# Performance work log

Measured on AMD Instinct MI355X. Metric: run time of the kernel, lower is better.

## Reference

```python
import jax, jax.numpy as jnp
import numpy as np

LEAKY = 0.1

def _leaky(x):
    return jax.nn.leaky_relu(x, LEAKY)

def _gather(pts, idx):
    # pts: [B, M, C], idx: [B, N, K] -> [B, N, K, C]
    return jax.vmap(lambda p, i: p[i])(pts, idx)

def _cross(xyz1, xyz2, p1, p2, pos_w, pos_b, mlps, k):
    # xyz1:[B,N1,3] xyz2:[B,N2,3] p1:[B,N1,D] p2:[B,N2,D]
    d = (jnp.sum(xyz1 * xyz1, -1)[:, :, None]
         + jnp.sum(xyz2 * xyz2, -1)[:, None, :]
         - 2.0 * jnp.einsum('bnc,bmc->bnm', xyz1, xyz2))  # [B,N1,N2]
    _, idx = jax.lax.top_k(-d, k)                          # smallest-k -> [B,N1,K]
    nb_xyz = _gather(xyz2, idx)                            # [B,N1,K,3]
    direction = nb_xyz - xyz1[:, :, None, :]
    g2 = _gather(p2, idx)                                  # [B,N1,K,D]
    posf = direction @ pos_w.T + pos_b                     # 1x1 conv on 3->D
    x = _leaky(g2 + p1[:, :, None, :] + posf)              # bn = Identity
    for w, b in mlps:
        x = _leaky(x @ w.T + b)                            # 1x1 Conv2d + bias + leaky
    return jnp.max(x, axis=2)                              # max-pool over K -> [B,N1,Cout]

def setup_inputs() -> dict:
    key = jax.random.key(0)
    ks = jax.random.split(key, 24)
    B, N, C, M1, M2, K = 2, 8192, 64, 64, 64, 16
    s = 0.1
    inp = {
        'pc1': jax.random.normal(ks[0], (B, 3, N), jnp.float32),
        'pc2': jax.random.normal(ks[1], (B, 3, N), jnp.float32),
        'feat1': jax.random.normal(ks[2], (B, C, N), jnp.float32),
        'feat2': jax.random.normal(ks[3], (B, C, N), jnp.float32),
        't11_w': jax.random.normal(ks[4], (M1, C), jnp.float32) * s,
        't11_b': jax.random.normal(ks[5], (M1,), jnp.float32) * s,
        't22_w': jax.random.normal(ks[6], (M1, C), jnp.float32) * s,
        't22_b': jax.random.normal(ks[7], (M1,), jnp.float32) * s,
        'pos1_w': jax.random.normal(ks[8], (M1, 3), jnp.float32) * s,
        'pos1_b': jax.random.normal(ks[9], (M1,), jnp.float32) * s,
        'mlp1_w1': jax.random.normal(ks[10], (M1, M1), jnp.float32) * s,
        'mlp1_b1': jax.random.normal(ks[11], (M1,), jnp.float32) * s,
        'mlp1_w2': jax.random.normal(ks[12], (M1, M1), jnp.float32) * s,
        'mlp1_b2': jax.random.normal(ks[13], (M1,), jnp.float32) * s,
        't1_w': jax.random.normal(ks[14], (M2, M1), jnp.float32) * s,
        't1_b': jax.random.normal(ks[15], (M2,), jnp.float32) * s,
        't2_w': jax.random.normal(ks[16], (M2, M1), jnp.float32) * s,
        't2_b': jax.random.normal(ks[17], (M2,), jnp.float32) * s,
        'pos2_w': jax.random.normal(ks[18], (M2, 3), jnp.float32) * s,
        'pos2_b': jax.random.normal(ks[19], (M2,), jnp.float32) * s,
        'mlp2_w1': jax.random.normal(ks[20], (M2, M2), jnp.float32) * s,
        'mlp2_b1': jax.random.normal(ks[21], (M2,), jnp.float32) * s,
    }
    return inp

def reference(pc1, pc2, feat1, feat2,
              t11_w, t11_b, t22_w, t22_b,
              pos1_w, pos1_b, mlp1_w1, mlp1_b1, mlp1_w2, mlp1_b2,
              t1_w, t1_b, t2_w, t2_b,
              pos2_w, pos2_b, mlp2_w1, mlp2_b1):
    K = 16
    x1 = jnp.transpose(pc1, (0, 2, 1))    # [B,N,3]
    x2 = jnp.transpose(pc2, (0, 2, 1))
    f1 = jnp.transpose(feat1, (0, 2, 1))  # [B,N,C]
    f2 = jnp.transpose(feat2, (0, 2, 1))
    mlp1 = [(mlp1_w1, mlp1_b1), (mlp1_w2, mlp1_b2)]
    mlp2 = [(mlp2_w1, mlp2_b1)]
    # feat1_new = cross_t1(cross(pc1, pc2, t11(feat1), t22(feat2), pos1, mlp1))
    q1 = f1 @ t11_w.T + t11_b
    q2 = f2 @ t22_w.T + t22_b
    fn1 = _cross(x1, x2, q1, q2, pos1_w, pos1_b, mlp1, K) @ t1_w.T + t1_b  # [B,N,M2]
    # feat2_new = cross_t2(cross(pc2, pc1, t11(feat2), t22(feat1), pos1, mlp1))
    r1 = f2 @ t11_w.T + t11_b
    r2 = f1 @ t22_w.T + t22_b
    fn2 = _cross(x2, x1, r1, r2, pos1_w, pos1_b, mlp1, K) @ t2_w.T + t2_b  # [B,N,M2]
    # feat1_final = cross(pc1, pc2, feat1_new, feat2_new, pos2, mlp2)
    ff = _cross(x1, x2, fn1, fn2, pos2_w, pos2_b, mlp2, K)                 # [B,N,M2]
    to_cn = lambda a: jnp.transpose(a, (0, 2, 1))  # back to [B,C,N] torch layout
    return (to_cn(fn1), to_cn(fn2), to_cn(ff))
```

## Files before the change

kernel.cpp:

```cpp
#include <hip/hip_runtime.h>

#define NPTS 8192
#define BATCH 2
#define CC 64
#define KNN 16

typedef __attribute__((ext_vector_type(4))) float  f32x4;
typedef __attribute__((ext_vector_type(8))) short  s16x8;
typedef unsigned short u16;

__device__ __forceinline__ u16 f2bf(float f) {
  unsigned u = __float_as_uint(f);
  unsigned r = ((u >> 16) & 1u) + 0x7FFFu;
  return (u16)((u + r) >> 16);
}

__device__ __forceinline__ float leaky(float v) { return fmaxf(v, 0.1f * v); }

__device__ __forceinline__ s16x8 pack8(const float v[8]) {
  union { s16x8 v8; u16 s[8]; } u;
  #pragma unroll
  for (int j = 0; j < 8; ++j) u.s[j] = f2bf(v[j]);
  return u.v8;
}

__global__ __launch_bounds__(256) void kprep(const float* __restrict__ pc1,
                                             const float* __restrict__ pc2,
                                             float4* __restrict__ x1t,
                                             float4* __restrict__ x2t) {
  int i = blockIdx.x * 256 + threadIdx.x;
  int b = i >> 13, n = i & (NPTS - 1);
  size_t base = (size_t)b * 3 * NPTS + n;
  float x = pc1[base], y = pc1[base + NPTS], z = pc1[base + 2 * NPTS];
  x1t[i] = make_float4(x, y, z, x * x + y * y + z * z);
  x = pc2[base]; y = pc2[base + NPTS]; z = pc2[base + 2 * NPTS];
  x2t[i] = make_float4(x, y, z, x * x + y * y + z * z);
}

__global__ __launch_bounds__(256) void ktrans(
    const float* __restrict__ f1, const float* __restrict__ f2,
    const float* __restrict__ w11, const float* __restrict__ b11,
    const float* __restrict__ w22, const float* __restrict__ b22,
    float* __restrict__ q1, float* __restrict__ q2,
    float* __restrict__ r1, float* __restrict__ r2) {
  const int z = blockIdx.z;
  const float* in = (z == 0 || z == 3) ? f1 : f2;
  const float* W  = (z == 0 || z == 2) ? w11 : w22;
  const float* Bb = (z == 0 || z == 2) ? b11 : b22;
  float* out = (z == 0) ? q1 : (z == 1) ? q2 : (z == 2) ? r1 : r2;
  const int b = blockIdx.y;
  const int n0 = blockIdx.x * 64;
  const int t = threadIdx.x;

  __shared__ float ft[64 * 65];
  __shared__ float wt[64 * 68];

  #pragma unroll
  for (int j = 0; j < 16; ++j) {
    int e = t + 256 * j;
    int c = e >> 6, tn = e & 63;
    ft[c * 65 + tn] = in[((size_t)b * 64 + c) * NPTS + n0 + tn];
  }
  #pragma unroll
  for (int j = 0; j < 16; ++j) {
    int e = t + 256 * j;
    int mm = e >> 6, c = e & 63;
    wt[c * 68 + mm] = W[e];
  }
  __syncthreads();

  const int tn = t & 63, mg = t >> 6;
  float a[16];
  #pragma unroll
  for (int u = 0; u < 4; ++u) {
    float4 bb = *(const float4*)&Bb[16 * mg + 4 * u];
    a[4 * u] = bb.x; a[4 * u + 1] = bb.y; a[4 * u + 2] = bb.z; a[4 * u + 3] = bb.w;
  }
  for (int c = 0; c < 64; ++c) {
    float x = ft[c * 65 + tn];
    #pragma unroll
    for (int u = 0; u < 4; ++u) {
      float4 w4 = *(const float4*)&wt[c * 68 + 16 * mg + 4 * u];
      a[4 * u]     = fmaf(x, w4.x, a[4 * u]);
      a[4 * u + 1] = fmaf(x, w4.y, a[4 * u + 1]);
      a[4 * u + 2] = fmaf(x, w4.z, a[4 * u + 2]);
      a[4 * u + 3] = fmaf(x, w4.w, a[4 * u + 3]);
    }
  }
  size_t ob = ((size_t)b * NPTS + n0 + tn) * 64 + 16 * mg;
  #pragma unroll
  for (int u = 0; u < 4; ++u)
    *(float4*)&out[ob + 4 * u] =
        make_float4(a[4 * u], a[4 * u + 1], a[4 * u + 2], a[4 * u + 3]);
}

__device__ __forceinline__ void kinsert(unsigned key, unsigned ii,
                                        unsigned (&D)[16], unsigned (&I)[16]) {
  if (key < D[15]) {
    bool lt[16];
    #pragma unroll
    for (int j = 0; j < 16; ++j) lt[j] = key < D[j];
    #pragma unroll
    for (int j = 15; j >= 1; --j) {
      D[j] = lt[j - 1] ? D[j - 1] : (lt[j] ? key : D[j]);
      I[j] = lt[j - 1] ? I[j - 1] : (lt[j] ? ii  : I[j]);
    }
    if (lt[0]) { D[0] = key; I[0] = ii; }
  }
}

#define CHUNKS 8
#define CHSZ (NPTS / CHUNKS)
#define NCOLD 2

#define ARD 20
#define ART 12

__global__ __launch_bounds__(256) void kknnA(const float4* __restrict__ x1t,
                                             const float4* __restrict__ x2t,
                                             uint2* __restrict__ part) {
  const int dir = blockIdx.z;
  const int b = blockIdx.y;
  const float4* xq = dir ? x2t : x1t;
  const float4* xc = dir ? x1t : x2t;
  const int t = threadIdx.x;
  const int qb = blockIdx.x & 31;
  const int ck = blockIdx.x >> 5;
  const int qi = qb * 256 + t;

  __shared__ float4 tile[CHSZ];
  __shared__ uint2 ring[ARD][256];

  const float4* src = xc + (size_t)b * NPTS + ck * CHSZ;
  #pragma unroll
  for (int j = 0; j < CHSZ / 256; ++j) tile[j * 256 + t] = src[j * 256 + t];

  float4 Q = xq[(size_t)b * NPTS + qi];
  const float nqx = -2.f * Q.x, nqy = -2.f * Q.y, nqz = -2.f * Q.z, qn = Q.w;

  unsigned D[16], I[16];
  #pragma unroll
  for (int j = 0; j < 16; ++j) { D[j] = 0xFFFFFFFFu; I[j] = 0u; }

  __syncthreads();

  const unsigned ibase = (unsigned)(ck * CHSZ);
  #pragma unroll
  for (int j = 0; j < 16; ++j) {
    float4 C = tile[j];
    float d = fmaf(C.x, nqx, fmaf(C.y, nqy, fmaf(C.z, nqz, qn + C.w)));
    unsigned key = (unsigned)max((int)__float_as_uint(d), 0);
    kinsert(key, ibase + j, D, I);
  }

  int cnt = 0;
  for (int j0 = 16; j0 < CHSZ; j0 += 8) {
    unsigned D15 = D[15];
    #pragma unroll
    for (int u = 0; u < 8; ++u) {
      float4 C = tile[j0 + u];
      float d = fmaf(C.x, nqx, fmaf(C.y, nqy, fmaf(C.z, nqz, qn + C.w)));
      unsigned key = (unsigned)max((int)__float_as_uint(d), 0);
      ring[cnt][t] = make_uint2(key, ibase + j0 + u);
      cnt += (key < D15) ? 1 : 0;
    }
    if (__any(cnt >= ART)) {
      for (int e = 0; e < cnt; ++e) {
        uint2 kv = ring[e][t];
        kinsert(kv.x, kv.y, D, I);
      }
      cnt = 0;
    }
  }
  for (int e = 0; e < cnt; ++e) {
    uint2 kv = ring[e][t];
    kinsert(kv.x, kv.y, D, I);
  }

  uint2* pb = part + ((size_t)(((dir << 1) | b) * CHUNKS + ck) * 16) * NPTS;
  #pragma unroll
  for (int j = 0; j < 16; ++j)
    pb[(size_t)j * NPTS + qi] = make_uint2(D[j], I[j]);
}

#define BRD 24
#define BRT 16

__global__ __launch_bounds__(256) void kknnB(const float4* __restrict__ x1t,
                                             const float4* __restrict__ x2t,
                                             uint2* __restrict__ part) {
  const int dir = blockIdx.z;
  const int b = blockIdx.y;
  const float4* xq = dir ? x2t : x1t;
  const float4* xc = dir ? x1t : x2t;
  const int t = threadIdx.x;
  const int qb = blockIdx.x & 31;
  const int ck = NCOLD + (blockIdx.x >> 5);
  const int qi = qb * 256 + t;

  __shared__ float4 tile[CHSZ];
  __shared__ u16 ring[BRD][256];

  const float4* src = xc + (size_t)b * NPTS + ck * CHSZ;
  #pragma unroll
  for (int j = 0; j < CHSZ / 256; ++j) tile[j * 256 + t] = src[j * 256 + t];

  float4 Q = xq[(size_t)b * NPTS + qi];
  const float nqx = -2.f * Q.x, nqy = -2.f * Q.y, nqz = -2.f * Q.z, qn = Q.w;

  const size_t gb = (size_t)(((dir << 1) | b) * CHUNKS) * 16 * NPTS;
  unsigned ta = part[gb + (size_t)15 * NPTS + qi].x;
  unsigned tb = part[gb + (size_t)(16 + 15) * NPTS + qi].x;
  const unsigned tfB = min(ta, tb) + 1u;

  unsigned D[16], I[16];
  #pragma unroll
  for (int j = 0; j < 16; ++j) { D[j] = 0xFFFFFFFFu; I[j] = 0u; }
  int cnt = 0;

  __syncthreads();

  const unsigned ibase = (unsigned)(ck * CHSZ);
  for (int j0 = 0; j0 < CHSZ; j0 += 8) {
    unsigned w = min(D[15], tfB);
    #pragma unroll
    for (int u = 0; u < 8; ++u) {
      float4 C = tile[j0 + u];
      float d = fmaf(C.x, nqx, fmaf(C.y, nqy, fmaf(C.z, nqz, qn + C.w)));
      unsigned key = (unsigned)max((int)__float_as_uint(d), 0);
      ring[cnt][t] = (u16)(j0 + u);
      cnt += (key < w) ? 1 : 0;
    }
    if (__any(cnt >= BRT)) {
      for (int e = 0; e < cnt; ++e) {
        int ji = ring[e][t];
        float4 C = tile[ji];
        float d = fmaf(C.x, nqx, fmaf(C.y, nqy, fmaf(C.z, nqz, qn + C.w)));
        unsigned key = (unsigned)max((int)__float_as_uint(d), 0);
        kinsert(key, ibase + ji, D, I);
      }
      cnt = 0;
    }
  }
  for (int e = 0; e < cnt; ++e) {
    int ji = ring[e][t];
    float4 C = tile[ji];
    float d = fmaf(C.x, nqx, fmaf(C.y, nqy, fmaf(C.z, nqz, qn + C.w)));
    unsigned key = (unsigned)max((int)__float_as_uint(d), 0);
    kinsert(key, ibase + ji, D, I);
  }

  uint2* pb = part + ((size_t)(((dir << 1) | b) * CHUNKS + ck) * 16) * NPTS;
  #pragma unroll
  for (int j = 0; j < 16; ++j)
    pb[(size_t)j * NPTS + qi] = make_uint2(D[j], I[j]);
}

__global__ __launch_bounds__(256) void kmerge(const uint2* __restrict__ part,
                                              int* __restrict__ idx12,
                                              int* __restrict__ idx21) {
  const int dir = blockIdx.z, b = blockIdx.y;
  const int qi = blockIdx.x * 256 + threadIdx.x;
  const uint2* pb = part + ((size_t)(((dir << 1) | b) * CHUNKS) * 16) * NPTS;

  unsigned D[16], I[16];
  #pragma unroll
  for (int j = 0; j < 16; ++j) {
    uint2 kv = pb[(size_t)j * NPTS + qi];
    D[j] = kv.x; I[j] = kv.y;
  }
  for (int ck = 1; ck < CHUNKS; ++ck) {
    #pragma unroll
    for (int j = 0; j < 16; ++j) {
      uint2 kv = pb[(size_t)(ck * 16 + j) * NPTS + qi];
      kinsert(kv.x, kv.y, D, I);
    }
  }
  int* out = dir ? idx21 : idx12;
  size_t ob = ((size_t)b * NPTS + qi) * 16;
  #pragma unroll
  for (int j = 0; j < 16; ++j) out[ob + j] = (int)I[j];
}

template <int NL>
__global__ __launch_bounds__(256) void kcross(
    const float4* __restrict__ xq0, const float4* __restrict__ xc0, const int* __restrict__ idx0,
    const float* __restrict__ p10, const float* __restrict__ p20,
    float* __restrict__ orm0, float* __restrict__ ocn0,
    const float4* __restrict__ xq1, const float4* __restrict__ xc1, const int* __restrict__ idx1,
    const float* __restrict__ p11, const float* __restrict__ p21,
    float* __restrict__ orm1, float* __restrict__ ocn1,
    const float* __restrict__ posw, const float* __restrict__ posb,
    const float* __restrict__ w1, const float* __restrict__ b1,
    const float* __restrict__ w2, const float* __restrict__ b2) {
  const float4* xq; const float4* xc; const int* idx; const float* p1; const float* p2;
  float* orm; float* ocn;
  if (blockIdx.y == 0) { xq = xq0; xc = xc0; idx = idx0; p1 = p10; p2 = p20; orm = orm0; ocn = ocn0; }
  else                 { xq = xq1; xc = xc1; idx = idx1; p1 = p11; p2 = p21; orm = orm1; ocn = ocn1; }

  __shared__ float4 pw4[64];
  __shared__ __align__(16) u16 ylds[4][16 * 72];

  const int t = threadIdx.x;
  const int lane = t & 63;
  const int w = t >> 6;
  const int m = lane & 15;
  const int q = lane >> 4;

  if (t < 64) pw4[t] = make_float4(posw[t * 3], posw[t * 3 + 1], posw[t * 3 + 2], posb[t]);
  __syncthreads();

  s16x8 wf[2][4][2];
  float bv[2][4];
  #pragma unroll
  for (int l = 0; l < NL; ++l) {
    const float* Wl = l ? w2 : w1;
    const float* Bl = l ? b2 : b1;
    #pragma unroll
    for (int ct = 0; ct < 4; ++ct) {
      bv[l][ct] = Bl[16 * ct + m];
      const float* rowp = Wl + (size_t)(16 * ct + m) * 64;
      #pragma unroll
      for (int kt = 0; kt < 2; ++kt) {
        const float* pp = rowp + 32 * kt + 8 * q;
        float4 A  = *(const float4*)pp;
        float4 Bq = *(const float4*)(pp + 4);
        float vv[8] = {A.x, A.y, A.z, A.w, Bq.x, Bq.y, Bq.z, Bq.w};
        wf[l][ct][kt] = pack8(vv);
      }
    }
  }

  u16* yw = &ylds[w][0];
  const f32x4 zz = {0.f, 0.f, 0.f, 0.f};

  #pragma unroll 1
  for (int i = 0; i < 4; ++i) {
    int gp = blockIdx.x * 16 + w * 4 + i;
    int b = gp >> 13, n = gp & (NPTS - 1);
    size_t qb = (size_t)b * NPTS + n;
    int nb = idx[qb * 16 + m];
    size_t cb = (size_t)b * NPTS + nb;
    float4 qp  = xq[qb];
    float4 nbp = xc[cb];
    float dx = nbp.x - qp.x, dy = nbp.y - qp.y, dz = nbp.z - qp.z;

    s16x8 af[2];
    #pragma unroll
    for (int h = 0; h < 2; ++h) {
      int c0 = 32 * h + 8 * q;
      const float* g2p = p2 + cb * 64 + c0;
      float4 ga = *(const float4*)g2p;
      float4 gb = *(const float4*)(g2p + 4);
      const float* p1p = p1 + qb * 64 + c0;
      float4 pa = *(const float4*)p1p;
      float4 pb = *(const float4*)(p1p + 4);
      float gg[8] = {ga.x + pa.x, ga.y + pa.y, ga.z + pa.z, ga.w + pa.w,
                     gb.x + pb.x, gb.y + pb.y, gb.z + pb.z, gb.w + pb.w};
      float vv[8];
      #pragma unroll
      for (int j = 0; j < 8; ++j) {
        float4 pw = pw4[c0 + j];
        float v = gg[j] + pw.w;
        v = fmaf(dx, pw.x, v);
        v = fmaf(dy, pw.y, v);
        v = fmaf(dz, pw.z, v);
        vv[j] = leaky(v);
      }
      af[h] = pack8(vv);
    }

    f32x4 acc[4];
    #pragma unroll
    for (int ct = 0; ct < 4; ++ct) {
      acc[ct] = __builtin_amdgcn_mfma_f32_16x16x32_bf16(af[0], wf[0][ct][0], zz, 0, 0, 0);
      acc[ct] = __builtin_amdgcn_mfma_f32_16x16x32_bf16(af[1], wf[0][ct][1], acc[ct], 0, 0, 0);
    }
    float y[4][4];
    #pragma unroll
    for (int ct = 0; ct < 4; ++ct)
      #pragma unroll
      for (int r = 0; r < 4; ++r)
        y[ct][r] = leaky(acc[ct][r] + bv[0][ct]);

    if (NL == 2) {
      #pragma unroll
      for (int ct = 0; ct < 4; ++ct)
        #pragma unroll
        for (int r = 0; r < 4; ++r)
          yw[(q * 4 + r) * 72 + 16 * ct + m] = f2bf(y[ct][r]);
      asm volatile("s_waitcnt lgkmcnt(0)" ::: "memory");
      s16x8 a2[2];
      a2[0] = *(const s16x8*)(yw + m * 72 + 8 * q);
      a2[1] = *(const s16x8*)(yw + m * 72 + 32 + 8 * q);
      #pragma unroll
      for (int ct = 0; ct < 4; ++ct) {
        acc[ct] = __builtin_amdgcn_mfma_f32_16x16x32_bf16(a2[0], wf[1][ct][0], zz, 0, 0, 0);
        acc[ct] = __builtin_amdgcn_mfma_f32_16x16x32_bf16(a2[1], wf[1][ct][1], acc[ct], 0, 0, 0);
      }
      #pragma unroll
      for (int ct = 0; ct < 4; ++ct)
        #pragma unroll
        for (int r = 0; r < 4; ++r)
          y[ct][r] = leaky(acc[ct][r] + bv[1][ct]);
      asm volatile("s_waitcnt lgkmcnt(0)" ::: "memory");
    }

    float pm[4];
    #pragma unroll
    for (int ct = 0; ct < 4; ++ct) {
      float v = fmaxf(fmaxf(y[ct][0], y[ct][1]), fmaxf(y[ct][2], y[ct][3]));
      v = fmaxf(v, __shfl_xor(v, 16));
      v = fmaxf(v, __shfl_xor(v, 32));
      pm[ct] = v;
    }
    float sel = (q == 0) ? pm[0] : (q == 1) ? pm[1] : (q == 2) ? pm[2] : pm[3];
    if (orm) orm[qb * 64 + lane] = sel;
    if (ocn) ocn[((size_t)b * 64 + lane) * NPTS + n] = sel;
  }
}

__global__ __launch_bounds__(256) void kpost(
    const float* __restrict__ inA, const float* __restrict__ inB,
    const float* __restrict__ wA, const float* __restrict__ bA,
    const float* __restrict__ wB, const float* __restrict__ bB,
    float* __restrict__ frA, float* __restrict__ frB,
    float* __restrict__ cnA, float* __restrict__ cnB) {
  const int z = blockIdx.z;
  const float* in = z ? inB : inA;
  const float* W  = z ? wB : wA;
  const float* Bb = z ? bB : bA;
  float* fr = z ? frB : frA;
  float* cn = z ? cnB : cnA;
  const int b = blockIdx.y;
  const int n0 = blockIdx.x * 64;
  const int t = threadIdx.x;

  __shared__ float pl[64 * 65];
  __shared__ float wt[64 * 68];

  #pragma unroll
  for (int j = 0; j < 16; ++j) {
    int e = t + 256 * j;
    int r = e >> 6, c = e & 63;
    pl[r * 65 + c] = in[((size_t)b * NPTS + n0 + r) * 64 + c];
  }
  #pragma unroll
  for (int j = 0; j < 16; ++j) {
    int e = t + 256 * j;
    int mm = e >> 6, c = e & 63;
    wt[c * 68 + mm] = W[e];
  }
  __syncthreads();

  const int tn = t & 63, mg = t >> 6;
  float a[16];
  #pragma unroll
  for (int u = 0; u < 4; ++u) {
    float4 bb = *(const float4*)&Bb[16 * mg + 4 * u];
    a[4 * u] = bb.x; a[4 * u + 1] = bb.y; a[4 * u + 2] = bb.z; a[4 * u + 3] = bb.w;
  }
  for (int c = 0; c < 64; ++c) {
    float x = pl[tn * 65 + c];
    #pragma unroll
    for (int u = 0; u < 4; ++u) {
      float4 w4 = *(const float4*)&wt[c * 68 + 16 * mg + 4 * u];
      a[4 * u]     = fmaf(x, w4.x, a[4 * u]);
      a[4 * u + 1] = fmaf(x, w4.y, a[4 * u + 1]);
      a[4 * u + 2] = fmaf(x, w4.z, a[4 * u + 2]);
      a[4 * u + 3] = fmaf(x, w4.w, a[4 * u + 3]);
    }
  }
  size_t ob = ((size_t)b * NPTS + n0 + tn) * 64 + 16 * mg;
  #pragma unroll
  for (int u = 0; u < 4; ++u)
    *(float4*)&fr[ob + 4 * u] =
        make_float4(a[4 * u], a[4 * u + 1], a[4 * u + 2], a[4 * u + 3]);
  #pragma unroll
  for (int jj = 0; jj < 16; ++jj) {
    int mo = 16 * mg + jj;
    cn[((size_t)b * 64 + mo) * NPTS + n0 + tn] = a[jj];
  }
}

extern "C" void kernel_launch(void* const* d_in, const int* in_sizes, int n_in,
                              void* d_out, int out_size, void* d_ws, size_t ws_size,
                              hipStream_t stream) {
  const float* pc1   = (const float*)d_in[0];
  const float* pc2   = (const float*)d_in[1];
  const float* feat1 = (const float*)d_in[2];
  const float* feat2 = (const float*)d_in[3];
  const float* t11w  = (const float*)d_in[4];
  const float* t11b  = (const float*)d_in[5];
  const float* t22w  = (const float*)d_in[6];
  const float* t22b  = (const float*)d_in[7];
  const float* pos1w = (const float*)d_in[8];
  const float* pos1b = (const float*)d_in[9];
  const float* m1w1  = (const float*)d_in[10];
  const float* m1b1  = (const float*)d_in[11];
  const float* m1w2  = (const float*)d_in[12];
  const float* m1b2  = (const float*)d_in[13];
  const float* t1w   = (const float*)d_in[14];
  const float* t1b   = (const float*)d_in[15];
  const float* t2w   = (const float*)d_in[16];
  const float* t2b   = (const float*)d_in[17];
  const float* pos2w = (const float*)d_in[18];
  const float* pos2b = (const float*)d_in[19];
  const float* m2w1  = (const float*)d_in[20];
  const float* m2b1  = (const float*)d_in[21];

  char* ws = (char*)d_ws;
  size_t off = 0;
  auto take = [&](size_t bytes) {
    char* p = ws + off;
    off += (bytes + 255) & ~(size_t)255;
    return p;
  };
  float4* x1t  = (float4*)take((size_t)BATCH * NPTS * sizeof(float4));
  float4* x2t  = (float4*)take((size_t)BATCH * NPTS * sizeof(float4));
  int* idx12   = (int*)take((size_t)BATCH * NPTS * KNN * 4);
  int* idx21   = (int*)take((size_t)BATCH * NPTS * KNN * 4);
  float* q1    = (float*)take((size_t)BATCH * NPTS * CC * 4);
  float* q2    = (float*)take((size_t)BATCH * NPTS * CC * 4);
  float* r1    = (float*)take((size_t)BATCH * NPTS * CC * 4);
  float* r2    = (float*)take((size_t)BATCH * NPTS * CC * 4);
  float* poolA = (float*)take((size_t)BATCH * NPTS * CC * 4);
  float* poolB = (float*)take((size_t)BATCH * NPTS * CC * 4);
  float* fn1   = (float*)take((size_t)BATCH * NPTS * CC * 4);
  float* fn2   = (float*)take((size_t)BATCH * NPTS * CC * 4);
  take((size_t)2 * 1024 * 1024);
  uint2* part  = (uint2*)q1;

  float* out = (float*)d_out;
  size_t seg = (size_t)BATCH * CC * NPTS;

  kprep<<<dim3(BATCH * NPTS / 256), 256, 0, stream>>>(pc1, pc2, x1t, x2t);
  kknnA<<<dim3(32 * NCOLD, BATCH, 2), 256, 0, stream>>>(x1t, x2t, part);
  kknnB<<<dim3(32 * (CHUNKS - NCOLD), BATCH, 2), 256, 0, stream>>>(x1t, x2t, part);
  kmerge<<<dim3(NPTS / 256, BATCH, 2), 256, 0, stream>>>(part, idx12, idx21);
  ktrans<<<dim3(NPTS / 64, BATCH, 4), 256, 0, stream>>>(
      feat1, feat2, t11w, t11b, t22w, t22b, q1, q2, r1, r2);
  kcross<2><<<dim3(1024, 2), 256, 0, stream>>>(
      x1t, x2t, idx12, q1, q2, poolA, (float*)nullptr,
      x2t, x1t, idx21, r1, r2, poolB, (float*)nullptr,
      pos1w, pos1b, m1w1, m1b1, m1w2, m1b2);
  kpost<<<dim3(NPTS / 64, BATCH, 2), 256, 0, stream>>>(
      poolA, poolB, t1w, t1b, t2w, t2b, fn1, fn2, out, out + seg);
  kcross<1><<<dim3(1024, 1), 256, 0, stream>>>(
      x1t, x2t, idx12, fn1, fn2, (float*)nullptr, out + 2 * seg,
      x1t, x2t, idx12, fn1, fn2, (float*)nullptr, (float*)nullptr,
      pos2w, pos2b, m2w1, m2b1, m2w1, m2b1);
}
```

Before: 463.6 us.

## Split cold KNN pass into smaller sub-chunks and stage final cross output via LDS

The first-pass KNN now uses four 512-point sub-chunks instead of two 1024-point chunks, and drops the serial 16-insert warmup. The second pass covers the remaining six 1024-point chunks and filters with a threshold taken from the minimum of four cold lists. The goal is more parallelism in the latency-bound cold pass at the cost of more partial lists for the merge to read. Separately, the final cross kernel stages its channel-major output in shared memory so it can write coalesced float4 stores instead of scattered scalars.

```diff
diff --git a/kernel.cpp b/kernel.cpp
--- a/kernel.cpp
+++ b/kernel.cpp
@@ -109,14 +109,78 @@
   }
 }
 
-#define CHUNKS 8
-#define CHSZ (NPTS / CHUNKS)
-#define NCOLD 2
-
-#define ARD 20
-#define ART 12
+#define ASUB 4
+#define ASZ 512
+#define WCH 6
+#define WSZ 1024
+#define NLISTS (ASUB + WCH)
+
+#define ARD 24
+#define ART 16
 
 __global__ __launch_bounds__(256) void kknnA(const float4* __restrict__ x1t,
+                                             const float4* __restrict__ x2t,
+                                             uint2* __restrict__ part) {
+  const int dir = blockIdx.z;
+  const int b = blockIdx.y;
+  const float4* xq = dir ? x2t : x1t;
+  const float4* xc = dir ? x1t : x2t;
+  const int t = threadIdx.x;
+  const int qb = blockIdx.x & 31;
+  const int sc = blockIdx.x >> 5;
+  const int qi = qb * 256 + t;
+
+  __shared__ float4 tile[ASZ];
+  __shared__ uint2 ring[ARD][256];
+
+  const float4* src = xc + (size_t)b * NPTS + sc * ASZ;
+  #pragma unroll
+  for (int j = 0; j < ASZ / 256; ++j) tile[j * 256 + t] = src[j * 256 + t];
+
+  float4 Q = xq[(size_t)b * NPTS + qi];
+  const float nqx = -2.f * Q.x, nqy = -2.f * Q.y, nqz = -2.f * Q.z, qn = Q.w;
+
+  unsigned D[16], I[16];
+  #pragma unroll
+  for (int j = 0; j < 16; ++j) { D[j] = 0xFFFFFFFFu; I[j] = 0u; }
+  int cnt = 0;
+
+  __syncthreads();
+
+  const unsigned ibase = (unsigned)(sc * ASZ);
+  for (int j0 = 0; j0 < ASZ; j0 += 8) {
+    unsigned D15 = D[15];
+    #pragma unroll
+    for (int u = 0; u < 8; ++u) {
+      float4 C = tile[j0 + u];
+      float d = fmaf(C.x, nqx, fmaf(C.y, nqy, fmaf(C.z, nqz, qn + C.w)));
+      unsigned key = (unsigned)max((int)__float_as_uint(d), 0);
+      ring[cnt][t] = make_uint2(key, ibase + j0 + u);
+      cnt += (key < D15) ? 1 : 0;
+    }
+    if (__any(cnt >= ART)) {
+      for (int e = 0; e < cnt; ++e) {
+        uint2 kv = ring[e][t];
+        kinsert(kv.x, kv.y, D, I);
+      }
+      cnt = 0;
+    }
+  }
+  for (int e = 0; e < cnt; ++e) {
+    uint2 kv = ring[e][t];
+    kinsert(kv.x, kv.y, D, I);
+  }
+
+  uint2* pb = part + ((size_t)(((dir << 1) | b) * NLISTS + sc) * 16) * NPTS;
+  #pragma unroll
+  for (int j = 0; j < 16; ++j)
+    pb[(size_t)j * NPTS + qi] = make_uint2(D[j], I[j]);
+}
+
+#define BRD 24
+#define BRT 16
+
+__global__ __launch_bounds__(256) void kknnB(const float4* __restrict__ x1t,
                                              const float4* __restrict__ x2t,
                                              uint2* __restrict__ part) {
   const int dir = blockIdx.z;
@@ -127,91 +191,24 @@
   const int qb = blockIdx.x & 31;
   const int ck = blockIdx.x >> 5;
   const int qi = qb * 256 + t;
-
-  __shared__ float4 tile[CHSZ];
-  __shared__ uint2 ring[ARD][256];
-
-  const float4* src = xc + (size_t)b * NPTS + ck * CHSZ;
-  #pragma unroll
-  for (int j = 0; j < CHSZ / 256; ++j) tile[j * 256 + t] = src[j * 256 + t];
+  const int cbase = ASUB * ASZ + ck * WSZ;
+
+  __shared__ float4 tile[WSZ];
+  __shared__ u16 ring[BRD][256];
+
+  const float4* src = xc + (size_t)b * NPTS + cbase;
+  #pragma unroll
+  for (int j = 0; j < WSZ / 256; ++j) tile[j * 256 + t] = src[j * 256 + t];
 
   float4 Q = xq[(size_t)b * NPTS + qi];
   const float nqx = -2.f * Q.x, nqy = -2.f * Q.y, nqz = -2.f * Q.z, qn = Q.w;
 
-  unsigned D[16], I[16];
-  #pragma unroll
-  for (int j = 0; j < 16; ++j) { D[j] = 0xFFFFFFFFu; I[j] = 0u; }
-
-  __syncthreads();
-
-  const unsigned ibase = (unsigned)(ck * CHSZ);
-  #pragma unroll
-  for (int j = 0; j < 16; ++j) {
-    float4 C = tile[j];
-    float d = fmaf(C.x, nqx, fmaf(C.y, nqy, fmaf(C.z, nqz, qn + C.w)));
-    unsigned key = (unsigned)max((int)__float_as_uint(d), 0);
-    kinsert(key, ibase + j, D, I);
-  }
-
-  int cnt = 0;
-  for (int j0 = 16; j0 < CHSZ; j0 += 8) {
-    unsigned D15 = D[15];
-    #pragma unroll
-    for (int u = 0; u < 8; ++u) {
-      float4 C = tile[j0 + u];
-      float d = fmaf(C.x, nqx, fmaf(C.y, nqy, fmaf(C.z, nqz, qn + C.w)));
-      unsigned key = (unsigned)max((int)__float_as_uint(d), 0);
-      ring[cnt][t] = make_uint2(key, ibase + j0 + u);
-      cnt += (key < D15) ? 1 : 0;
-    }
-    if (__any(cnt >= ART)) {
-      for (int e = 0; e < cnt; ++e) {
-        uint2 kv = ring[e][t];
-        kinsert(kv.x, kv.y, D, I);
-      }
-      cnt = 0;
-    }
-  }
-  for (int e = 0; e < cnt; ++e) {
-    uint2 kv = ring[e][t];
-    kinsert(kv.x, kv.y, D, I);
-  }
-
-  uint2* pb = part + ((size_t)(((dir << 1) | b) * CHUNKS + ck) * 16) * NPTS;
-  #pragma unroll
-  for (int j = 0; j < 16; ++j)
-    pb[(size_t)j * NPTS + qi] = make_uint2(D[j], I[j]);
-}
-
-#define BRD 24
-#define BRT 16
-
-__global__ __launch_bounds__(256) void kknnB(const float4* __restrict__ x1t,
-                                             const float4* __restrict__ x2t,
-                                             uint2* __restrict__ part) {
-  const int dir = blockIdx.z;
-  const int b = blockIdx.y;
-  const float4* xq = dir ? x2t : x1t;
-  const float4* xc = dir ? x1t : x2t;
-  const int t = threadIdx.x;
-  const int qb = blockIdx.x & 31;
-  const int ck = NCOLD + (blockIdx.x >> 5);
-  const int qi = qb * 256 + t;
-
-  __shared__ float4 tile[CHSZ];
-  __shared__ u16 ring[BRD][256];
-
-  const float4* src = xc + (size_t)b * NPTS + ck * CHSZ;
-  #pragma unroll
-  for (int j = 0; j < CHSZ / 256; ++j) tile[j * 256 + t] = src[j * 256 + t];
-
-  float4 Q = xq[(size_t)b * NPTS + qi];
-  const float nqx = -2.f * Q.x, nqy = -2.f * Q.y, nqz = -2.f * Q.z, qn = Q.w;
-
-  const size_t gb = (size_t)(((dir << 1) | b) * CHUNKS) * 16 * NPTS;
-  unsigned ta = part[gb + (size_t)15 * NPTS + qi].x;
-  unsigned tb = part[gb + (size_t)(16 + 15) * NPTS + qi].x;
-  const unsigned tfB = min(ta, tb) + 1u;
+  const size_t gb = (size_t)(((dir << 1) | b) * NLISTS) * 16 * NPTS;
+  unsigned tm = part[gb + (size_t)15 * NPTS + qi].x;
+  #pragma unroll
+  for (int s = 1; s < ASUB; ++s)
+    tm = min(tm, part[gb + (size_t)(s * 16 + 15) * NPTS + qi].x);
+  const unsigned tfB = tm + 1u;
 
   unsigned D[16], I[16];
   #pragma unroll
@@ -220,8 +217,8 @@
 
   __syncthreads();
 
-  const unsigned ibase = (unsigned)(ck * CHSZ);
-  for (int j0 = 0; j0 < CHSZ; j0 += 8) {
+  const unsigned ibase = (unsigned)cbase;
+  for (int j0 = 0; j0 < WSZ; j0 += 8) {
     unsigned w = min(D[15], tfB);
     #pragma unroll
     for (int u = 0; u < 8; ++u) {
@@ -250,7 +247,7 @@
     kinsert(key, ibase + ji, D, I);
   }
 
-  uint2* pb = part + ((size_t)(((dir << 1) | b) * CHUNKS + ck) * 16) * NPTS;
+  uint2* pb = part + ((size_t)(((dir << 1) | b) * NLISTS + ASUB + ck) * 16) * NPTS;
   #pragma unroll
   for (int j = 0; j < 16; ++j)
     pb[(size_t)j * NPTS + qi] = make_uint2(D[j], I[j]);
@@ -261,7 +258,7 @@
                                               int* __restrict__ idx21) {
   const int dir = blockIdx.z, b = blockIdx.y;
   const int qi = blockIdx.x * 256 + threadIdx.x;
-  const uint2* pb = part + ((size_t)(((dir << 1) | b) * CHUNKS) * 16) * NPTS;
+  const uint2* pb = part + ((size_t)(((dir << 1) | b) * NLISTS) * 16) * NPTS;
 
   unsigned D[16], I[16];
   #pragma unroll
@@ -269,10 +266,10 @@
     uint2 kv = pb[(size_t)j * NPTS + qi];
     D[j] = kv.x; I[j] = kv.y;
   }
-  for (int ck = 1; ck < CHUNKS; ++ck) {
+  for (int l = 1; l < NLISTS; ++l) {
     #pragma unroll
     for (int j = 0; j < 16; ++j) {
-      uint2 kv = pb[(size_t)(ck * 16 + j) * NPTS + qi];
+      uint2 kv = pb[(size_t)(l * 16 + j) * NPTS + qi];
       kinsert(kv.x, kv.y, D, I);
     }
   }
@@ -300,6 +297,7 @@
 
   __shared__ float4 pw4[64];
   __shared__ __align__(16) u16 ylds[4][16 * 72];
+  __shared__ float otile[16][68];
 
   const int t = threadIdx.x;
   const int lane = t & 63;
@@ -416,7 +414,18 @@
     }
     float sel = (q == 0) ? pm[0] : (q == 1) ? pm[1] : (q == 2) ? pm[2] : pm[3];
     if (orm) orm[qb * 64 + lane] = sel;
-    if (ocn) ocn[((size_t)b * 64 + lane) * NPTS + n] = sel;
+    if (ocn) otile[w * 4 + i][lane] = sel;
+  }
+
+  if (ocn) {
+    __syncthreads();
+    int gp0 = blockIdx.x * 16;
+    int b = gp0 >> 13, n0 = gp0 & (NPTS - 1);
+    int ch = t >> 2;
+    int nn = (t & 3) * 4;
+    float4 v = make_float4(otile[nn][ch], otile[nn + 1][ch],
+                           otile[nn + 2][ch], otile[nn + 3][ch]);
+    *(float4*)&ocn[((size_t)b * 64 + ch) * NPTS + n0 + nn] = v;
   }
 }
 
@@ -528,15 +537,15 @@
   float* poolB = (float*)take((size_t)BATCH * NPTS * CC * 4);
   float* fn1   = (float*)take((size_t)BATCH * NPTS * CC * 4);
   float* fn2   = (float*)take((size_t)BATCH * NPTS * CC * 4);
-  take((size_t)2 * 1024 * 1024);
+  take((size_t)10 * 1024 * 1024);
   uint2* part  = (uint2*)q1;
 
   float* out = (float*)d_out;
   size_t seg = (size_t)BATCH * CC * NPTS;
 
   kprep<<<dim3(BATCH * NPTS / 256), 256, 0, stream>>>(pc1, pc2, x1t, x2t);
-  kknnA<<<dim3(32 * NCOLD, BATCH, 2), 256, 0, stream>>>(x1t, x2t, part);
-  kknnB<<<dim3(32 * (CHUNKS - NCOLD), BATCH, 2), 256, 0, stream>>>(x1t, x2t, part);
+  kknnA<<<dim3(32 * ASUB, BATCH, 2), 256, 0, stream>>>(x1t, x2t, part);
+  kknnB<<<dim3(32 * WCH, BATCH, 2), 256, 0, stream>>>(x1t, x2t, part);
   kmerge<<<dim3(NPTS / 256, BATCH, 2), 256, 0, stream>>>(part, idx12, idx21);
   ktrans<<<dim3(NPTS / 64, BATCH, 4), 256, 0, stream>>>(
       feat1, feat2, t11w, t11b, t22w, t22b, q1, q2, r1, r2);
```

Result: no change. 465.4 us (+0.4%).
